# Kernel tuning notes

Measured on AMD Instinct MI355X. Metric: run time of the kernel, lower is better.

## Reference

```python
import jax, jax.numpy as jnp
import numpy as np

B, S, T = 4, 512, 512
D, F, L, H, V = 512, 2048, 6, 8, 32000
HD = D // H


def setup_inputs() -> dict:
    key = jax.random.key(0)
    ks = list(jax.random.split(key, 16))
    it = iter(ks)

    def w(shape, scale=0.02):
        return jax.random.normal(next(it), shape, jnp.float32) * scale

    enc_in = jax.random.randint(next(it), (B, S), 0, V, dtype=jnp.int32)
    dec_in = jax.random.randint(next(it), (B, T), 0, V, dtype=jnp.int32)

    # sinusoidal positional encoding (make_sine_pos_encoding)
    pos = np.arange(S)[:, None].astype(np.float32)
    i = np.arange(D)[None, :].astype(np.float32)
    angle = pos / np.power(10000.0, (2.0 * np.floor(i / 2.0)) / D)
    pe = np.zeros((S, D), np.float32)
    pe[:, 0::2] = np.sin(angle[:, 0::2])
    pe[:, 1::2] = np.cos(angle[:, 1::2])

    return {
        "enc_in": enc_in,
        "dec_in": dec_in,
        "e_embed": w((V, D)),
        "d_embed": w((V, D)),
        "pos_enc": jnp.asarray(pe),
        "enc_mha_W": w((L, 4, D, D)),      # q,k,v,out
        "enc_mha_b": jnp.zeros((L, 4, D), jnp.float32),
        "enc_ln_g": jnp.ones((L, 2, D), jnp.float32),
        "enc_ln_b": jnp.zeros((L, 2, D), jnp.float32),
        "enc_ffn_W1": w((L, D, F)),
        "enc_ffn_b1": jnp.zeros((L, F), jnp.float32),
        "enc_ffn_W2": w((L, F, D)),
        "enc_ffn_b2": jnp.zeros((L, D), jnp.float32),
        "dec_mha_W": w((L, 8, D, D)),      # self q,k,v,out then cross q,k,v,out
        "dec_mha_b": jnp.zeros((L, 8, D), jnp.float32),
        "dec_ln_g": jnp.ones((L, 3, D), jnp.float32),
        "dec_ln_b": jnp.zeros((L, 3, D), jnp.float32),
        "dec_ffn_W1": w((L, D, F)),
        "dec_ffn_b1": jnp.zeros((L, F), jnp.float32),
        "dec_ffn_W2": w((L, F, D)),
        "dec_ffn_b2": jnp.zeros((L, D), jnp.float32),
    }


def _layer_norm(x, g, b, eps=1e-6):
    m = jnp.mean(x, axis=-1, keepdims=True)
    v = jnp.mean(jnp.square(x - m), axis=-1, keepdims=True)
    return (x - m) * jax.lax.rsqrt(v + eps) * g + b


def _split_heads(x):
    b, n, _ = x.shape
    return x.reshape(b, n, H, HD).transpose(0, 2, 1, 3)  # b h n d


def _mha(xq, xkv, W, b, mask):
    # W: [>=4, D, D] slice of (q,k,v,out); mask: broadcastable to [b,h,nq,nk]
    q = _split_heads(xq @ W[0] + b[0])
    k = _split_heads(xkv @ W[1] + b[1])
    v = _split_heads(xkv @ W[2] + b[2])
    s = jnp.einsum('bhqd,bhkd->bhqk', q, k) / jnp.sqrt(jnp.float32(HD))
    s = s + mask * (-1e9)
    a = jax.nn.softmax(s, axis=-1)
    o = jnp.einsum('bhqk,bhkd->bhqd', a, v)
    o = o.transpose(0, 2, 1, 3).reshape(xq.shape[0], xq.shape[1], D)
    return o @ W[3] + b[3]


def _forward(enc_in, dec_in, e_embed, d_embed, pos_enc,
             enc_mha_W, enc_mha_b, enc_ln_g, enc_ln_b,
             enc_ffn_W1, enc_ffn_b1, enc_ffn_W2, enc_ffn_b2,
             dec_mha_W, dec_mha_b, dec_ln_g, dec_ln_b,
             dec_ffn_W1, dec_ffn_b1, dec_ffn_W2, dec_ffn_b2):
    # masks: 1.0 where attention is blocked
    enc_pad = (enc_in == 0).astype(jnp.float32)[:, None, None, :]   # [B,1,1,S]
    dec_pad = (dec_in == 0).astype(jnp.float32)[:, None, None, :]   # [B,1,1,T]
    la = jnp.triu(jnp.ones((T, T), jnp.float32), k=1)[None, None]   # [1,1,T,T]
    look_ahead = jnp.maximum(la, dec_pad)                           # [B,1,T,T]

    scale = jnp.float32(D) ** 0.5
    e = e_embed[enc_in] * scale + pos_enc[None, :S]
    d = d_embed[dec_in] * scale + pos_enc[None, :T]

    for l in range(L):
        y = _mha(e, e, enc_mha_W[l], enc_mha_b[l], enc_pad)
        e = _layer_norm(e + y, enc_ln_g[l, 0], enc_ln_b[l, 0])
        y = jax.nn.relu(e @ enc_ffn_W1[l] + enc_ffn_b1[l]) @ enc_ffn_W2[l] + enc_ffn_b2[l]
        e = _layer_norm(e + y, enc_ln_g[l, 1], enc_ln_b[l, 1])

    for l in range(L):
        y = _mha(d, d, dec_mha_W[l, 0:4], dec_mha_b[l, 0:4], look_ahead)
        d = _layer_norm(d + y, dec_ln_g[l, 0], dec_ln_b[l, 0])
        y = _mha(d, e, dec_mha_W[l, 4:8], dec_mha_b[l, 4:8], enc_pad)
        d = _layer_norm(d + y, dec_ln_g[l, 1], dec_ln_b[l, 1])
        y = jax.nn.relu(d @ dec_ffn_W1[l] + dec_ffn_b1[l]) @ dec_ffn_W2[l] + dec_ffn_b2[l]
        d = _layer_norm(d + y, dec_ln_g[l, 2], dec_ln_b[l, 2])

    return d @ d_embed.T  # [B,T,V] logits


def reference(enc_in, dec_in, e_embed, d_embed, pos_enc,
              enc_mha_W, enc_mha_b, enc_ln_g, enc_ln_b,
              enc_ffn_W1, enc_ffn_b1, enc_ffn_W2, enc_ffn_b2,
              dec_mha_W, dec_mha_b, dec_ln_g, dec_ln_b,
              dec_ffn_W1, dec_ffn_b1, dec_ffn_W2, dec_ffn_b2):
    return _forward(enc_in, dec_in, e_embed, d_embed, pos_enc,
                    enc_mha_W, enc_mha_b, enc_ln_g, enc_ln_b,
                    enc_ffn_W1, enc_ffn_b1, enc_ffn_W2, enc_ffn_b2,
                    dec_mha_W, dec_mha_b, dec_ln_g, dec_ln_b,
                    dec_ffn_W1, dec_ffn_b1, dec_ffn_W2, dec_ffn_b2)
```

## Files before the change

### kernel.cpp

```cpp
#include <hip/hip_runtime.h>
#include <hip/hip_bf16.h>
#include <math.h>

#define B_ 4
#define S_ 512
#define D_ 512
#define F_ 2048
#define L_ 6
#define H_ 8
#define V_ 32000

typedef unsigned short u16;
typedef __attribute__((ext_vector_type(8))) short bhalf8;
typedef __attribute__((ext_vector_type(4))) float f32x4;

__device__ __forceinline__ u16 f2b(float v) {
    unsigned x = __builtin_bit_cast(unsigned, v);
    return (u16)((x + 0x7FFFu + ((x >> 16) & 1u)) >> 16);
}

#define GLD16(g, l) __builtin_amdgcn_global_load_lds( \
    (const __attribute__((address_space(1))) void*)(g), \
    (__attribute__((address_space(3))) void*)(l), 16, 0, 0)

__device__ __forceinline__ float redmax16(float v) {
    #pragma unroll
    for (int m = 1; m < 16; m <<= 1) v = fmaxf(v, __shfl_xor(v, m));
    return v;
}
__device__ __forceinline__ float redsum16(float v) {
    #pragma unroll
    for (int m = 1; m < 16; m <<= 1) v += __shfl_xor(v, m);
    return v;
}

template<int NWR, int NWC, int WM, int WN, int OUT, int RELU, int MLOOP,
         int SPLITA, int XMAJOR, int NT, int VTT>
__global__ __launch_bounds__(NWR * NWC * 64)
void mfma_gemm(const u16* __restrict__ A, const u16* __restrict__ A2, int acut,
               const u16* __restrict__ B,
               const float* __restrict__ bias, void* __restrict__ Cv,
               int K, int lda, int ldb, int ldc,
               u16* __restrict__ vtp, int vc0)
{
    constexpr int BM = NWR * WM, BN = NWC * WN;
    constexpr int NW = NWR * NWC;
    constexpr int CH_A = BM / 16, CH_B = BN / 16, CH = CH_A + CH_B;
    constexpr int NI = WM / 16, NJ = WN / 16;

    __shared__ u16 As[BM * 32];
    __shared__ u16 Bs[BN * 32];
    __shared__ u16 TT[VTT ? 64 * 72 : 8];

    const int tid = threadIdx.x;
    const int wid = tid >> 6, lane = tid & 63;
    const int wrow = wid / NWC, wcol = wid % NWC;
    const long bn = (XMAJOR ? (long)blockIdx.y : (long)blockIdx.x) * BN;
    const long bmbase = (XMAJOR ? (long)blockIdx.x : (long)blockIdx.y);
    const int r4 = lane >> 2, c4 = lane & 3;
    const int l15 = lane & 15, l4 = lane >> 4;

    const u16* Ause = (SPLITA && bn >= acut) ? A2 : A;

    #pragma unroll 1
    for (int mi = 0; mi < MLOOP; ++mi) {
        const long bm = (bmbase * MLOOP + mi) * BM;

        f32x4 acc[NI][NJ];
        #pragma unroll
        for (int i = 0; i < NI; ++i)
            #pragma unroll
            for (int j = 0; j < NJ; ++j)
                acc[i][j] = (f32x4){0.f, 0.f, 0.f, 0.f};

        for (int k0 = 0; k0 < K; k0 += 32) {
            #pragma unroll
            for (int t = 0; t < CH / NW; ++t) {
                int c = wid + t * NW;
                if (c < CH_A) {
                    const u16* g = Ause + (bm + c * 16 + r4) * (long)lda + k0 + c4 * 8;
                    GLD16(g, As + c * 512 + lane * 8);
                } else {
                    int cb = c - CH_A;
                    const u16* g = B + (bn + cb * 16 + r4) * (long)ldb + k0 + c4 * 8;
                    GLD16(g, Bs + cb * 512 + lane * 8);
                }
            }
            __syncthreads();
            bhalf8 af[NI], bfr[NJ];
            #pragma unroll
            for (int i = 0; i < NI; ++i)
                af[i] = *(const bhalf8*)&As[(wrow * WM + i * 16 + l15) * 32 + l4 * 8];
            #pragma unroll
            for (int j = 0; j < NJ; ++j)
                bfr[j] = *(const bhalf8*)&Bs[(wcol * WN + j * 16 + l15) * 32 + l4 * 8];
            #pragma unroll
            for (int i = 0; i < NI; ++i)
                #pragma unroll
                for (int j = 0; j < NJ; ++j)
                    acc[i][j] = __builtin_amdgcn_mfma_f32_16x16x32_bf16(af[i], bfr[j], acc[i][j], 0, 0, 0);
            __syncthreads();
        }

        if (VTT && vtp != nullptr && bn >= vc0) {
            #pragma unroll
            for (int j = 0; j < NJ; ++j) {
                const int c = wcol * WN + j * 16 + l15;
                const float bv = bias ? bias[bn + c] : 0.f;
                #pragma unroll
                for (int i = 0; i < NI; ++i) {
                    const int rw = wrow * WM + i * 16 + (l4 << 2);
                    #pragma unroll
                    for (int r = 0; r < 4; ++r)
                        TT[c * 72 + rw + r] = f2b(acc[i][j][r] + bv);
                }
            }
            __syncthreads();
            {
                const int c = tid >> 1, hh = tid & 1;
                const u16* src = &TT[c * 72 + hh * 32];
                u16* dst = &vtp[(bn - vc0 + c) * 2048 + bm + hh * 32];
                #pragma unroll
                for (int p = 0; p < 4; ++p)
                    *(uint4*)(dst + p * 8) = *(const uint4*)(src + p * 8);
            }
            __syncthreads();
            continue;
        }

        float* Cf = (float*)Cv;
        u16*   Cb = (u16*)Cv;
        const int rowb = wrow * WM + (l4 << 2);
        const int colb = wcol * WN + l15;
        #pragma unroll
        for (int j = 0; j < NJ; ++j) {
            const long gc = bn + colb + j * 16;
            const float bv = bias ? bias[gc] : 0.f;
            #pragma unroll
            for (int i = 0; i < NI; ++i) {
                const long gr = bm + rowb + i * 16;
                #pragma unroll
                for (int r = 0; r < 4; ++r) {
                    float v = acc[i][j][r] + bv;
                    if (RELU) v = fmaxf(v, 0.f);
                    if (OUT == 0) {
                        if (NT) __builtin_nontemporal_store(v, &Cf[(gr + r) * (long)ldc + gc]);
                        else    Cf[(gr + r) * (long)ldc + gc] = v;
                    } else {
                        Cb[(gr + r) * (long)ldc + gc] = f2b(v);
                    }
                }
            }
        }
    }
}

__global__ __launch_bounds__(512)
void gemm_ln_kernel(const u16* __restrict__ A, const u16* __restrict__ B,
                    const float* __restrict__ bias,
                    float* __restrict__ x, u16* __restrict__ xb,
                    const float* __restrict__ g, const float* __restrict__ bb,
                    int K)
{
    __shared__ u16 As[16 * 32];
    __shared__ u16 Bs[512 * 32];
    __shared__ float red[2][16][8];
    __shared__ float mv[2][16];

    const int tid = threadIdx.x, w = tid >> 6, lane = tid & 63;
    const int l15 = lane & 15, l4 = lane >> 4;
    const int r4 = lane >> 2, c4 = lane & 3;
    const long bm = (long)blockIdx.x * 16;

    f32x4 acc[4];
    #pragma unroll
    for (int j = 0; j < 4; ++j) acc[j] = (f32x4){0.f, 0.f, 0.f, 0.f};

    for (int k0 = 0; k0 < K; k0 += 32) {
        #pragma unroll
        for (int t = 0; t < 5; ++t) {
            int c = w + t * 8;
            if (c < 33) {
                if (c == 0) {
                    GLD16(A + (bm + r4) * (long)K + k0 + c4 * 8, As + lane * 8);
                } else {
                    GLD16(B + ((c - 1) * 16 + r4) * (long)K + k0 + c4 * 8,
                          Bs + (c - 1) * 512 + lane * 8);
                }
            }
        }
        __syncthreads();
        bhalf8 af = *(const bhalf8*)&As[l15 * 32 + l4 * 8];
        #pragma unroll
        for (int j = 0; j < 4; ++j) {
            bhalf8 bf = *(const bhalf8*)&Bs[(w * 64 + j * 16 + l15) * 32 + l4 * 8];
            acc[j] = __builtin_amdgcn_mfma_f32_16x16x32_bf16(af, bf, acc[j], 0, 0, 0);
        }
        __syncthreads();
    }

    float vbuf[4][4], s[4] = {0, 0, 0, 0}, s2[4] = {0, 0, 0, 0};
    #pragma unroll
    for (int j = 0; j < 4; ++j) {
        int col = w * 64 + j * 16 + l15;
        float bv = bias[col];
        #pragma unroll
        for (int r = 0; r < 4; ++r) {
            int row = l4 * 4 + r;
            float v = acc[j][r] + bv + x[(bm + row) * 512 + col];
            vbuf[j][r] = v;
            s[r] += v; s2[r] += v * v;
        }
    }
    #pragma unroll
    for (int r = 0; r < 4; ++r) { s[r] = redsum16(s[r]); s2[r] = redsum16(s2[r]); }
    if (l15 == 0) {
        #pragma unroll
        for (int r = 0; r < 4; ++r) {
            red[0][l4 * 4 + r][w] = s[r];
            red[1][l4 * 4 + r][w] = s2[r];
        }
    }
    __syncthreads();
    if (tid < 16) {
        float S = 0.f, S2 = 0.f;
        #pragma unroll
        for (int q = 0; q < 8; ++q) { S += red[0][tid][q]; S2 += red[1][tid][q]; }
        float mean = S * (1.f / 512.f);
        float var = S2 * (1.f / 512.f) - mean * mean;
        mv[0][tid] = mean;
        mv[1][tid] = rsqrtf(var + 1e-6f);
    }
    __syncthreads();
    #pragma unroll
    for (int j = 0; j < 4; ++j) {
        int col = w * 64 + j * 16 + l15;
        float gg = g[col], bbv = bb[col];
        #pragma unroll
        for (int r = 0; r < 4; ++r) {
            int row = l4 * 4 + r;
            float o = (vbuf[j][r] - mv[0][row]) * mv[1][row] * gg + bbv;
            x[(bm + row) * 512 + col] = o;
            xb[(bm + row) * 512 + col] = f2b(o);
        }
    }
}

template<int CAUSAL>
__global__ __launch_bounds__(256)
void flash_kernel(const u16* __restrict__ Qp, int ldq,
                  const u16* __restrict__ Kp, int ldk,
                  const u16* __restrict__ Vt,
                  const int* __restrict__ tok,
                  u16* __restrict__ Op)
{
    __shared__ u16 QS[64 * 64];
    __shared__ u16 KS[64 * 64];
    __shared__ u16 VS[64 * 64];
    __shared__ u16 PS[4 * 16 * 64];
    __shared__ float MK[512];

    const int tid = threadIdx.x, lane = tid & 63, w = tid >> 6;
    const int l15 = lane & 15, l4 = lane >> 4;
    const int qb = blockIdx.x, bh = blockIdx.y;
    const int b = bh >> 3, h = bh & 7;

    const u16* Q = Qp + (long)(b * 512 + qb * 64) * ldq + h * 64;
    const u16* K = Kp + (long)(b * 512) * ldk + h * 64;
    const u16* V = Vt + (long)(h * 64) * 2048 + b * 512;
    u16* O = Op + (long)(b * 512 + qb * 64) * 512 + h * 64;

    {
        int t0 = tok[b * 512 + tid];
        int t1 = tok[b * 512 + 256 + tid];
        MK[tid]       = (t0 == 0) ? -1e9f : 0.f;
        MK[tid + 256] = (t1 == 0) ? -1e9f : 0.f;
    }
    {
        int r = tid >> 3;
        int c = (tid & 7) ^ (r & 7);
        GLD16(Q + (long)r * ldq + c * 8,        QS + tid * 8);
        GLD16(Q + (long)(r + 32) * ldq + c * 8, QS + 2048 + tid * 8);
    }

    f32x4 oacc[4];
    float mrun[4], lrun[4];
    #pragma unroll
    for (int j = 0; j < 4; ++j) oacc[j] = (f32x4){0.f, 0.f, 0.f, 0.f};
    #pragma unroll
    for (int r = 0; r < 4; ++r) { mrun[r] = -1e30f; lrun[r] = 0.f; }

    bhalf8 qa[2];
    const int tmax = CAUSAL ? qb : 7;

    for (int t = 0; t <= tmax; ++t) {
        {
            int r = tid >> 3;
            int c = (tid & 7) ^ (r & 7);
            GLD16(K + (long)(t * 64 + r) * ldk + c * 8,       KS + tid * 8);
            GLD16(K + (long)(t * 64 + 32 + r) * ldk + c * 8,  KS + 2048 + tid * 8);
            GLD16(V + (long)r * 2048 + t * 64 + c * 8,        VS + tid * 8);
            GLD16(V + (long)(r + 32) * 2048 + t * 64 + c * 8, VS + 2048 + tid * 8);
        }
        __syncthreads();
        if (t == 0) {
            #pragma unroll
            for (int kc = 0; kc < 2; ++kc) {
                int row = w * 16 + l15;
                qa[kc] = *(const bhalf8*)&QS[row * 64 + (((kc * 4 + l4) ^ (row & 7)) << 3)];
            }
        }
        f32x4 sac[4];
        #pragma unroll
        for (int jj = 0; jj < 4; ++jj) sac[jj] = (f32x4){0.f, 0.f, 0.f, 0.f};
        bhalf8 kf[4][2];
        #pragma unroll
        for (int jj = 0; jj < 4; ++jj)
            #pragma unroll
            for (int kc = 0; kc < 2; ++kc) {
                int row = jj * 16 + l15;
                kf[jj][kc] = *(const bhalf8*)&KS[row * 64 + (((kc * 4 + l4) ^ (row & 7)) << 3)];
            }
        #pragma unroll
        for (int jj = 0; jj < 4; ++jj)
            #pragma unroll
            for (int kc = 0; kc < 2; ++kc)
                sac[jj] = __builtin_amdgcn_mfma_f32_16x16x32_bf16(qa[kc], kf[jj][kc], sac[jj], 0, 0, 0);

        #pragma unroll
        for (int jj = 0; jj < 4; ++jj) {
            float mk = MK[t * 64 + jj * 16 + l15];
            #pragma unroll
            for (int r = 0; r < 4; ++r) {
                float mk2 = mk;
                if (CAUSAL && t == qb) {
                    int col = t * 64 + jj * 16 + l15;
                    int qr = qb * 64 + w * 16 + l4 * 4 + r;
                    if (col > qr) mk2 = -1e9f;
                }
                sac[jj][r] = sac[jj][r] * 0.125f + mk2;
            }
        }
        #pragma unroll
        for (int r = 0; r < 4; ++r) {
            float mx = fmaxf(fmaxf(sac[0][r], sac[1][r]), fmaxf(sac[2][r], sac[3][r]));
            mx = redmax16(mx);
            float mnew = fmaxf(mrun[r], mx);
            float alpha = __expf(mrun[r] - mnew);
            float sum = 0.f;
            int row_p = l4 * 4 + r;
            #pragma unroll
            for (int jj = 0; jj < 4; ++jj) {
                float pv = __expf(sac[jj][r] - mnew);
                sum += pv;
                int kv = jj * 16 + l15;
                PS[w * 1024 + row_p * 64 + ((((kv >> 3) ^ (row_p & 7)) << 3) | (kv & 7))] = f2b(pv);
            }
            sum = redsum16(sum);
            lrun[r] = lrun[r] * alpha + sum;
            mrun[r] = mnew;
            #pragma unroll
            for (int jd = 0; jd < 4; ++jd) oacc[jd][r] *= alpha;
        }
        bhalf8 pa[2], vf[4][2];
        #pragma unroll
        for (int kc = 0; kc < 2; ++kc) {
            int row = l15;
            pa[kc] = *(const bhalf8*)&PS[w * 1024 + row * 64 + (((kc * 4 + l4) ^ (row & 7)) << 3)];
        }
        #pragma unroll
        for (int jd = 0; jd < 4; ++jd)
            #pragma unroll
            for (int kc = 0; kc < 2; ++kc) {
                int row = jd * 16 + l15;
                vf[jd][kc] = *(const bhalf8*)&VS[row * 64 + (((kc * 4 + l4) ^ (row & 7)) << 3)];
            }
        #pragma unroll
        for (int jd = 0; jd < 4; ++jd)
            #pragma unroll
            for (int kc = 0; kc < 2; ++kc)
                oacc[jd] = __builtin_amdgcn_mfma_f32_16x16x32_bf16(pa[kc], vf[jd][kc], oacc[jd], 0, 0, 0);
        __syncthreads();
    }

    #pragma unroll
    for (int r = 0; r < 4; ++r) {
        float inv = 1.f / lrun[r];
        int row = w * 16 + l4 * 4 + r;
        #pragma unroll
        for (int jd = 0; jd < 4; ++jd)
            O[(long)row * 512 + jd * 16 + l15] = f2b(oacc[jd][r] * inv);
    }
}

__global__ __launch_bounds__(256)
void transpose_many(const float* __restrict__ inA, const float* __restrict__ inB,
                    int zsplit, int R, int C, u16* __restrict__ out)
{
    int z = blockIdx.z;
    const float* in = (z < zsplit) ? inA + (long)z * R * C
                                   : inB + (long)(z - zsplit) * R * C;
    u16* o = out + (long)z * R * C;
    __shared__ float tb[64][65];
    const int tr = blockIdx.y * 64, tc = blockIdx.x * 64;
    const int col = threadIdx.x & 63, r0 = threadIdx.x >> 6;
    #pragma unroll
    for (int p = 0; p < 16; ++p) {
        int row = r0 * 16 + p;
        tb[row][col] = in[(long)(tr + row) * C + tc + col];
    }
    __syncthreads();
    #pragma unroll
    for (int p = 0; p < 16; ++p) {
        int row = r0 * 16 + p;
        o[(long)(tc + row) * R + tr + col] = f2b(tb[col][row]);
    }
}

__global__ __launch_bounds__(256)
void convert_b16(const float4* __restrict__ in, u16* __restrict__ out, long n4)
{
    long i = (long)blockIdx.x * 256 + threadIdx.x;
    if (i >= n4) return;
    float4 v = in[i];
    uint2 p;
    p.x = (unsigned)f2b(v.x) | ((unsigned)f2b(v.y) << 16);
    p.y = (unsigned)f2b(v.z) | ((unsigned)f2b(v.w) << 16);
    *(uint2*)(out + i * 4) = p;
}

__global__ __launch_bounds__(256)
void embed_kernel(const int* __restrict__ tE, const int* __restrict__ tD,
                  const float* __restrict__ eE, const float* __restrict__ eD,
                  const float* __restrict__ pos,
                  float* __restrict__ xE, float* __restrict__ xD,
                  u16* __restrict__ bE, u16* __restrict__ bD, float scale)
{
    const int z = blockIdx.y;
    const int* tok = z ? tD : tE;
    const float* emb = z ? eD : eE;
    float* x = z ? xD : xE;
    u16* xb = z ? bD : bE;
    int row = blockIdx.x;
    int s = row & (S_ - 1);
    int t = tok[row];
    const float* er = emb + (long)t * D_;
    const float* pr = pos + (long)s * D_;
    float* o = x + (long)row * D_;
    u16*  ob = xb + (long)row * D_;
    int i = threadIdx.x;
    float v0 = er[i]       * scale + pr[i];
    float v1 = er[i + 256] * scale + pr[i + 256];
    o[i] = v0;        o[i + 256] = v1;
    ob[i] = f2b(v0);  ob[i + 256] = f2b(v1);
}

__global__ __launch_bounds__(256)
void add_ln_kernel(float* __restrict__ x, const float* __restrict__ y,
                   u16* __restrict__ xb,
                   const float* __restrict__ g, const float* __restrict__ bb)
{
    long row = blockIdx.x;
    float* xr = x + row * D_;
    u16* xo = xb + row * D_;
    const float* yr = y + row * D_;
    int t = threadIdx.x, t2 = t + 256;

    float r0 = xr[t] + yr[t];
    float r1 = xr[t2] + yr[t2];
    float s = r0 + r1;
    float s2 = r0 * r0 + r1 * r1;
    #pragma unroll
    for (int i = 1; i < 64; i <<= 1) {
        s  += __shfl_xor(s, i);
        s2 += __shfl_xor(s2, i);
    }
    __shared__ float rs[4], rs2[4];
    int wid = t >> 6;
    if ((t & 63) == 0) { rs[wid] = s; rs2[wid] = s2; }
    __syncthreads();
    s  = rs[0] + rs[1] + rs[2] + rs[3];
    s2 = rs2[0] + rs2[1] + rs2[2] + rs2[3];

    float mean = s * (1.f / D_);
    float var  = s2 * (1.f / D_) - mean * mean;
    float inv  = rsqrtf(var + 1e-6f);
    float o0 = (r0 - mean) * inv * g[t]  + bb[t];
    float o1 = (r1 - mean) * inv * g[t2] + bb[t2];
    xr[t] = o0;       xr[t2] = o1;
    xo[t] = f2b(o0);  xo[t2] = f2b(o1);
}

extern "C" void kernel_launch(void* const* d_in, const int* in_sizes, int n_in,
                              void* d_out, int out_size, void* d_ws, size_t ws_size,
                              hipStream_t stream)
{
    const int*   enc_in     = (const int*)  d_in[0];
    const int*   dec_in     = (const int*)  d_in[1];
    const float* e_embed    = (const float*)d_in[2];
    const float* d_embed    = (const float*)d_in[3];
    const float* pos_enc    = (const float*)d_in[4];
    const float* enc_mha_W  = (const float*)d_in[5];
    const float* enc_mha_b  = (const float*)d_in[6];
    const float* enc_ln_g   = (const float*)d_in[7];
    const float* enc_ln_b   = (const float*)d_in[8];
    const float* enc_ffn_W1 = (const float*)d_in[9];
    const float* enc_ffn_b1 = (const float*)d_in[10];
    const float* enc_ffn_W2 = (const float*)d_in[11];
    const float* enc_ffn_b2 = (const float*)d_in[12];
    const float* dec_mha_W  = (const float*)d_in[13];
    const float* dec_mha_b  = (const float*)d_in[14];
    const float* dec_ln_g   = (const float*)d_in[15];
    const float* dec_ln_b   = (const float*)d_in[16];
    const float* dec_ffn_W1 = (const float*)d_in[17];
    const float* dec_ffn_b1 = (const float*)d_in[18];
    const float* dec_ffn_W2 = (const float*)d_in[19];
    const float* dec_ffn_b2 = (const float*)d_in[20];
    float* out = (float*)d_out;

    const int  BS  = B_ * S_;
    const long BSD = (long)BS * D_;
    const long DD  = (long)D_ * D_;
    const long DF  = (long)D_ * F_;

    char* p = (char*)d_ws;
    auto alloc = [&](long bytes) { char* r = p; p += (bytes + 255) & ~255L; return r; };
    float* e    = (float*)alloc(BSD * 4);
    float* dd   = (float*)alloc(BSD * 4);
    float* y    = (float*)alloc(BSD * 4);
    u16*   eb   = (u16*)  alloc(BSD * 2);
    u16*   ddb  = (u16*)  alloc(BSD * 2);
    u16*   qkv  = (u16*)  alloc((long)BS * 1536 * 2);
    u16*   att  = (u16*)  alloc(BSD * 2);
    u16*   vt   = (u16*)  alloc(BSD * 2);
    u16*   ffnh = (u16*)  alloc((long)BS * F_ * 2);
    u16*   wEmb = (u16*)  alloc((long)V_ * D_ * 2);
    u16*   wMha = (u16*)  alloc(72 * DD * 2);
    u16*   wF1  = (u16*)  alloc(12 * DF * 2);
    u16*   wF2  = (u16*)  alloc(12 * DF * 2);

    transpose_many<<<dim3(8, 8, 72), 256, 0, stream>>>(enc_mha_W, dec_mha_W, 24, 512, 512, wMha);
    transpose_many<<<dim3(32, 8, 12), 256, 0, stream>>>(enc_ffn_W1, dec_ffn_W1, 6, 512, 2048, wF1);
    transpose_many<<<dim3(8, 32, 12), 256, 0, stream>>>(enc_ffn_W2, dec_ffn_W2, 6, 2048, 512, wF2);
    convert_b16<<<16000, 256, 0, stream>>>((const float4*)d_embed, wEmb, (long)V_ * D_ / 4);

    const float scale = sqrtf((float)D_);
    embed_kernel<<<dim3(BS, 2), 256, 0, stream>>>(enc_in, dec_in, e_embed, d_embed,
                                                  pos_enc, e, dd, eb, ddb, scale);

    #define GEMM_BIG(grid, RELU, OUTT, A, Bp, bias, C, K, lda, ldb, ldc) \
        mfma_gemm<2,2,64,64,OUTT,RELU,1,0,0,0,0><<<grid, 256, 0, stream>>>(A, A, 1 << 30, Bp, bias, C, K, lda, ldb, ldc, nullptr, 0)
    #define GEMM_SKV(grid, A, Bp, bias, C, K, lda, ldb, ldc, vtp, vc0) \
        mfma_gemm<2,1,32,64,1,0,1,0,0,0,1><<<grid, 128, 0, stream>>>(A, A, 1 << 30, Bp, bias, C, K, lda, ldb, ldc, vtp, vc0)
    #define GEMM_SK(grid, OUTT, A, Bp, bias, C, K, lda, ldb, ldc) \
        mfma_gemm<2,1,32,64,OUTT,0,1,0,0,0,0><<<grid, 128, 0, stream>>>(A, A, 1 << 30, Bp, bias, C, K, lda, ldb, ldc, nullptr, 0)

    for (int l = 0; l < L_; ++l) {
        const u16* Wl = wMha + (long)l * 4 * DD;
        const float* bl = enc_mha_b + (long)l * 4 * D_;
        GEMM_SKV(dim3(24, 32), eb, Wl, bl, qkv, 512, 512, 512, 1536, vt, 1024);
        flash_kernel<0><<<dim3(8, 32), 256, 0, stream>>>(qkv, 1536, qkv + 512, 1536, vt, enc_in, att);
        gemm_ln_kernel<<<128, 512, 0, stream>>>(att, Wl + 3 * DD, bl + 3 * D_,
            e, eb, enc_ln_g + (long)(l * 2) * D_, enc_ln_b + (long)(l * 2) * D_, 512);
        GEMM_BIG(dim3(16, 16), 1, 1, eb, wF1 + (long)l * DF, enc_ffn_b1 + (long)l * F_,
                 ffnh, 512, 512, 512, 2048);
        GEMM_SK(dim3(8, 32), 0, ffnh, wF2 + (long)l * DF, enc_ffn_b2 + (long)l * D_,
                y, 2048, 2048, 2048, 512);
        add_ln_kernel<<<BS, 256, 0, stream>>>(e, y, eb,
            enc_ln_g + (long)(l * 2 + 1) * D_, enc_ln_b + (long)(l * 2 + 1) * D_);
    }

    for (int l = 0; l < L_; ++l) {
        const u16* Wl = wMha + (long)(24 + l * 8) * DD;
        const float* bl = dec_mha_b + (long)l * 8 * D_;
        GEMM_SKV(dim3(24, 32), ddb, Wl, bl, qkv, 512, 512, 512, 1536, vt, 1024);
        flash_kernel<1><<<dim3(8, 32), 256, 0, stream>>>(qkv, 1536, qkv + 512, 1536, vt, dec_in, att);
        gemm_ln_kernel<<<128, 512, 0, stream>>>(att, Wl + 3 * DD, bl + 3 * D_,
            dd, ddb, dec_ln_g + (long)(l * 3) * D_, dec_ln_b + (long)(l * 3) * D_, 512);
        mfma_gemm<2,1,32,64,1,0,1,1,0,0,1><<<dim3(24, 32), 128, 0, stream>>>(
            ddb, eb, 512, Wl + 4 * DD, bl + 4 * D_, qkv,
            512, 512, 512, 1536, vt, 1024);
        flash_kernel<0><<<dim3(8, 32), 256, 0, stream>>>(qkv, 1536, qkv + 512, 1536, vt, enc_in, att);
        gemm_ln_kernel<<<128, 512, 0, stream>>>(att, Wl + 7 * DD, bl + 7 * D_,
            dd, ddb, dec_ln_g + (long)(l * 3 + 1) * D_, dec_ln_b + (long)(l * 3 + 1) * D_, 512);
        GEMM_BIG(dim3(16, 16), 1, 1, ddb, wF1 + (long)(6 + l) * DF, dec_ffn_b1 + (long)l * F_,
                 ffnh, 512, 512, 512, 2048);
        GEMM_SK(dim3(8, 32), 0, ffnh, wF2 + (long)(6 + l) * DF, dec_ffn_b2 + (long)l * D_,
                y, 2048, 2048, 2048, 512);
        add_ln_kernel<<<BS, 256, 0, stream>>>(dd, y, ddb,
            dec_ln_g + (long)(l * 3 + 2) * D_, dec_ln_b + (long)(l * 3 + 2) * D_);
    }

    mfma_gemm<2,2,64,64,0,0,1,0,1,1,0><<<dim3(16, 250), 256, 0, stream>>>(
        ddb, ddb, 1 << 30, wEmb, nullptr, out, 512, 512, 512, 32000, nullptr, 0);
}
```

Measured before the change: 1.805 ms.

## Double-buffer LDS tiles in GEMM and flash attention; swizzle logits GEMM grid

Both the generic MFMA GEMM and the flash-attention kernel now use two LDS buffers. The next K tile (or next K/V block) is fetched with global_load_lds while MFMAs run on the current one, which removes one barrier per iteration and overlaps loads with compute. The final vocab-projection GEMM moves to a 1D grid with an XCD-aware swizzle that maps consecutive blocks onto shared N tiles, aiming to improve L2 reuse of embedding rows across the 8 XCDs. The cost is doubled LDS usage, which may reduce occupancy. Correctness relies on the single barrier per iteration ordering the reads of the previous buffer before it is overwritten.

```diff
diff --git a/kernel.cpp b/kernel.cpp
--- a/kernel.cpp
+++ b/kernel.cpp
@@ -35,7 +35,7 @@
 }
 
 template<int NWR, int NWC, int WM, int WN, int OUT, int RELU, int MLOOP,
-         int SPLITA, int XMAJOR, int NT, int VTT>
+         int SPLITA, int XMAJOR, int NT, int VTT, int SWZ>
 __global__ __launch_bounds__(NWR * NWC * 64)
 void mfma_gemm(const u16* __restrict__ A, const u16* __restrict__ A2, int acut,
                const u16* __restrict__ B,
@@ -48,15 +48,24 @@
     constexpr int CH_A = BM / 16, CH_B = BN / 16, CH = CH_A + CH_B;
     constexpr int NI = WM / 16, NJ = WN / 16;
 
-    __shared__ u16 As[BM * 32];
-    __shared__ u16 Bs[BN * 32];
+    __shared__ u16 As[2][BM * 32];
+    __shared__ u16 Bs[2][BN * 32];
     __shared__ u16 TT[VTT ? 64 * 72 : 8];
 
     const int tid = threadIdx.x;
     const int wid = tid >> 6, lane = tid & 63;
     const int wrow = wid / NWC, wcol = wid % NWC;
-    const long bn = (XMAJOR ? (long)blockIdx.y : (long)blockIdx.x) * BN;
-    const long bmbase = (XMAJOR ? (long)blockIdx.x : (long)blockIdx.y);
+    long bn, bmbase;
+    if (SWZ) {
+        long b0 = blockIdx.x;
+        long per = (long)gridDim.x >> 3;
+        long w = (b0 & 7) * per + (b0 >> 3);
+        bn = (w >> 4) * BN;
+        bmbase = w & 15;
+    } else {
+        bn = (XMAJOR ? (long)blockIdx.y : (long)blockIdx.x) * BN;
+        bmbase = (XMAJOR ? (long)blockIdx.x : (long)blockIdx.y);
+    }
     const int r4 = lane >> 2, c4 = lane & 3;
     const int l15 = lane & 15, l4 = lane >> 4;
 
@@ -73,33 +82,49 @@
             for (int j = 0; j < NJ; ++j)
                 acc[i][j] = (f32x4){0.f, 0.f, 0.f, 0.f};
 
+        #pragma unroll
+        for (int t = 0; t < CH / NW; ++t) {
+            int c = wid + t * NW;
+            if (c < CH_A) {
+                GLD16(Ause + (bm + c * 16 + r4) * (long)lda + c4 * 8,
+                      &As[0][c * 512 + lane * 8]);
+            } else {
+                int cb = c - CH_A;
+                GLD16(B + (bn + cb * 16 + r4) * (long)ldb + c4 * 8,
+                      &Bs[0][cb * 512 + lane * 8]);
+            }
+        }
+
         for (int k0 = 0; k0 < K; k0 += 32) {
-            #pragma unroll
-            for (int t = 0; t < CH / NW; ++t) {
-                int c = wid + t * NW;
-                if (c < CH_A) {
-                    const u16* g = Ause + (bm + c * 16 + r4) * (long)lda + k0 + c4 * 8;
-                    GLD16(g, As + c * 512 + lane * 8);
-                } else {
-                    int cb = c - CH_A;
-                    const u16* g = B + (bn + cb * 16 + r4) * (long)ldb + k0 + c4 * 8;
-                    GLD16(g, Bs + cb * 512 + lane * 8);
+            const int cur = (k0 >> 5) & 1;
+            __syncthreads();
+            if (k0 + 32 < K) {
+                const int kn = k0 + 32;
+                #pragma unroll
+                for (int t = 0; t < CH / NW; ++t) {
+                    int c = wid + t * NW;
+                    if (c < CH_A) {
+                        GLD16(Ause + (bm + c * 16 + r4) * (long)lda + kn + c4 * 8,
+                              &As[cur ^ 1][c * 512 + lane * 8]);
+                    } else {
+                        int cb = c - CH_A;
+                        GLD16(B + (bn + cb * 16 + r4) * (long)ldb + kn + c4 * 8,
+                              &Bs[cur ^ 1][cb * 512 + lane * 8]);
+                    }
                 }
             }
-            __syncthreads();
             bhalf8 af[NI], bfr[NJ];
             #pragma unroll
             for (int i = 0; i < NI; ++i)
-                af[i] = *(const bhalf8*)&As[(wrow * WM + i * 16 + l15) * 32 + l4 * 8];
+                af[i] = *(const bhalf8*)&As[cur][(wrow * WM + i * 16 + l15) * 32 + l4 * 8];
             #pragma unroll
             for (int j = 0; j < NJ; ++j)
-                bfr[j] = *(const bhalf8*)&Bs[(wcol * WN + j * 16 + l15) * 32 + l4 * 8];
+                bfr[j] = *(const bhalf8*)&Bs[cur][(wcol * WN + j * 16 + l15) * 32 + l4 * 8];
             #pragma unroll
             for (int i = 0; i < NI; ++i)
                 #pragma unroll
                 for (int j = 0; j < NJ; ++j)
                     acc[i][j] = __builtin_amdgcn_mfma_f32_16x16x32_bf16(af[i], bfr[j], acc[i][j], 0, 0, 0);
-            __syncthreads();
         }
 
         if (VTT && vtp != nullptr && bn >= vc0) {
@@ -255,8 +280,8 @@
                   u16* __restrict__ Op)
 {
     __shared__ u16 QS[64 * 64];
-    __shared__ u16 KS[64 * 64];
-    __shared__ u16 VS[64 * 64];
+    __shared__ u16 KS[2][64 * 64];
+    __shared__ u16 VS[2][64 * 64];
     __shared__ u16 PS[4 * 16 * 64];
     __shared__ float MK[512];
 
@@ -276,11 +301,23 @@
         MK[tid]       = (t0 == 0) ? -1e9f : 0.f;
         MK[tid + 256] = (t1 == 0) ? -1e9f : 0.f;
     }
+    const int r = tid >> 3;
+    const int c = (tid & 7) ^ (r & 7);
     {
-        int r = tid >> 3;
-        int c = (tid & 7) ^ (r & 7);
         GLD16(Q + (long)r * ldq + c * 8,        QS + tid * 8);
         GLD16(Q + (long)(r + 32) * ldq + c * 8, QS + 2048 + tid * 8);
+        GLD16(K + (long)r * ldk + c * 8,              KS[0] + tid * 8);
+        GLD16(K + (long)(32 + r) * ldk + c * 8,       KS[0] + 2048 + tid * 8);
+        GLD16(V + (long)r * 2048 + c * 8,             VS[0] + tid * 8);
+        GLD16(V + (long)(r + 32) * 2048 + c * 8,      VS[0] + 2048 + tid * 8);
+    }
+    __syncthreads();
+
+    bhalf8 qa[2];
+    #pragma unroll
+    for (int kc = 0; kc < 2; ++kc) {
+        int row = w * 16 + l15;
+        qa[kc] = *(const bhalf8*)&QS[row * 64 + (((kc * 4 + l4) ^ (row & 7)) << 3)];
     }
 
     f32x4 oacc[4];
@@ -288,27 +325,18 @@
     #pragma unroll
     for (int j = 0; j < 4; ++j) oacc[j] = (f32x4){0.f, 0.f, 0.f, 0.f};
     #pragma unroll
-    for (int r = 0; r < 4; ++r) { mrun[r] = -1e30f; lrun[r] = 0.f; }
-
-    bhalf8 qa[2];
+    for (int rr = 0; rr < 4; ++rr) { mrun[rr] = -1e30f; lrun[rr] = 0.f; }
+
     const int tmax = CAUSAL ? qb : 7;
 
     for (int t = 0; t <= tmax; ++t) {
-        {
-            int r = tid >> 3;
-            int c = (tid & 7) ^ (r & 7);
-            GLD16(K + (long)(t * 64 + r) * ldk + c * 8,       KS + tid * 8);
-            GLD16(K + (long)(t * 64 + 32 + r) * ldk + c * 8,  KS + 2048 + tid * 8);
-            GLD16(V + (long)r * 2048 + t * 64 + c * 8,        VS + tid * 8);
-            GLD16(V + (long)(r + 32) * 2048 + t * 64 + c * 8, VS + 2048 + tid * 8);
-        }
-        __syncthreads();
-        if (t == 0) {
-            #pragma unroll
-            for (int kc = 0; kc < 2; ++kc) {
-                int row = w * 16 + l15;
-                qa[kc] = *(const bhalf8*)&QS[row * 64 + (((kc * 4 + l4) ^ (row & 7)) << 3)];
-            }
+        const int cur = t & 1;
+        if (t < tmax) {
+            const int tn = t + 1;
+            GLD16(K + (long)(tn * 64 + r) * ldk + c * 8,        KS[cur ^ 1] + tid * 8);
+            GLD16(K + (long)(tn * 64 + 32 + r) * ldk + c * 8,   KS[cur ^ 1] + 2048 + tid * 8);
+            GLD16(V + (long)r * 2048 + tn * 64 + c * 8,         VS[cur ^ 1] + tid * 8);
+            GLD16(V + (long)(r + 32) * 2048 + tn * 64 + c * 8,  VS[cur ^ 1] + 2048 + tid * 8);
         }
         f32x4 sac[4];
         #pragma unroll
@@ -319,7 +347,7 @@
             #pragma unroll
             for (int kc = 0; kc < 2; ++kc) {
                 int row = jj * 16 + l15;
-                kf[jj][kc] = *(const bhalf8*)&KS[row * 64 + (((kc * 4 + l4) ^ (row & 7)) << 3)];
+                kf[jj][kc] = *(const bhalf8*)&KS[cur][row * 64 + (((kc * 4 + l4) ^ (row & 7)) << 3)];
             }
         #pragma unroll
         for (int jj = 0; jj < 4; ++jj)
@@ -331,36 +359,36 @@
         for (int jj = 0; jj < 4; ++jj) {
             float mk = MK[t * 64 + jj * 16 + l15];
             #pragma unroll
-            for (int r = 0; r < 4; ++r) {
+            for (int rr = 0; rr < 4; ++rr) {
                 float mk2 = mk;
                 if (CAUSAL && t == qb) {
                     int col = t * 64 + jj * 16 + l15;
-                    int qr = qb * 64 + w * 16 + l4 * 4 + r;
+                    int qr = qb * 64 + w * 16 + l4 * 4 + rr;
                     if (col > qr) mk2 = -1e9f;
                 }
-                sac[jj][r] = sac[jj][r] * 0.125f + mk2;
-            }
-        }
-        #pragma unroll
-        for (int r = 0; r < 4; ++r) {
-            float mx = fmaxf(fmaxf(sac[0][r], sac[1][r]), fmaxf(sac[2][r], sac[3][r]));
+                sac[jj][rr] = sac[jj][rr] * 0.125f + mk2;
+            }
+        }
+        #pragma unroll
+        for (int rr = 0; rr < 4; ++rr) {
+            float mx = fmaxf(fmaxf(sac[0][rr], sac[1][rr]), fmaxf(sac[2][rr], sac[3][rr]));
             mx = redmax16(mx);
-            float mnew = fmaxf(mrun[r], mx);
-            float alpha = __expf(mrun[r] - mnew);
+            float mnew = fmaxf(mrun[rr], mx);
+            float alpha = __expf(mrun[rr] - mnew);
             float sum = 0.f;
-            int row_p = l4 * 4 + r;
+            int row_p = l4 * 4 + rr;
             #pragma unroll
             for (int jj = 0; jj < 4; ++jj) {
-                float pv = __expf(sac[jj][r] - mnew);
+                float pv = __expf(sac[jj][rr] - mnew);
                 sum += pv;
                 int kv = jj * 16 + l15;
                 PS[w * 1024 + row_p * 64 + ((((kv >> 3) ^ (row_p & 7)) << 3) | (kv & 7))] = f2b(pv);
             }
             sum = redsum16(sum);
-            lrun[r] = lrun[r] * alpha + sum;
-            mrun[r] = mnew;
-            #pragma unroll
-            for (int jd = 0; jd < 4; ++jd) oacc[jd][r] *= alpha;
+            lrun[rr] = lrun[rr] * alpha + sum;
+            mrun[rr] = mnew;
+            #pragma unroll
+            for (int jd = 0; jd < 4; ++jd) oacc[jd][rr] *= alpha;
         }
         bhalf8 pa[2], vf[4][2];
         #pragma unroll
@@ -373,7 +401,7 @@
             #pragma unroll
             for (int kc = 0; kc < 2; ++kc) {
                 int row = jd * 16 + l15;
-                vf[jd][kc] = *(const bhalf8*)&VS[row * 64 + (((kc * 4 + l4) ^ (row & 7)) << 3)];
+                vf[jd][kc] = *(const bhalf8*)&VS[cur][row * 64 + (((kc * 4 + l4) ^ (row & 7)) << 3)];
             }
         #pragma unroll
         for (int jd = 0; jd < 4; ++jd)
@@ -384,12 +412,12 @@
     }
 
     #pragma unroll
-    for (int r = 0; r < 4; ++r) {
-        float inv = 1.f / lrun[r];
-        int row = w * 16 + l4 * 4 + r;
+    for (int rr = 0; rr < 4; ++rr) {
+        float inv = 1.f / lrun[rr];
+        int row = w * 16 + l4 * 4 + rr;
         #pragma unroll
         for (int jd = 0; jd < 4; ++jd)
-            O[(long)row * 512 + jd * 16 + l15] = f2b(oacc[jd][r] * inv);
+            O[(long)row * 512 + jd * 16 + l15] = f2b(oacc[jd][rr] * inv);
     }
 }
 
@@ -549,11 +577,11 @@
                                                   pos_enc, e, dd, eb, ddb, scale);
 
     #define GEMM_BIG(grid, RELU, OUTT, A, Bp, bias, C, K, lda, ldb, ldc) \
-        mfma_gemm<2,2,64,64,OUTT,RELU,1,0,0,0,0><<<grid, 256, 0, stream>>>(A, A, 1 << 30, Bp, bias, C, K, lda, ldb, ldc, nullptr, 0)
+        mfma_gemm<2,2,64,64,OUTT,RELU,1,0,0,0,0,0><<<grid, 256, 0, stream>>>(A, A, 1 << 30, Bp, bias, C, K, lda, ldb, ldc, nullptr, 0)
     #define GEMM_SKV(grid, A, Bp, bias, C, K, lda, ldb, ldc, vtp, vc0) \
-        mfma_gemm<2,1,32,64,1,0,1,0,0,0,1><<<grid, 128, 0, stream>>>(A, A, 1 << 30, Bp, bias, C, K, lda, ldb, ldc, vtp, vc0)
+        mfma_gemm<2,1,32,64,1,0,1,0,0,0,1,0><<<grid, 128, 0, stream>>>(A, A, 1 << 30, Bp, bias, C, K, lda, ldb, ldc, vtp, vc0)
     #define GEMM_SK(grid, OUTT, A, Bp, bias, C, K, lda, ldb, ldc) \
-        mfma_gemm<2,1,32,64,OUTT,0,1,0,0,0,0><<<grid, 128, 0, stream>>>(A, A, 1 << 30, Bp, bias, C, K, lda, ldb, ldc, nullptr, 0)
+        mfma_gemm<2,1,32,64,OUTT,0,1,0,0,0,0,0><<<grid, 128, 0, stream>>>(A, A, 1 << 30, Bp, bias, C, K, lda, ldb, ldc, nullptr, 0)
 
     for (int l = 0; l < L_; ++l) {
         const u16* Wl = wMha + (long)l * 4 * DD;
@@ -577,7 +605,7 @@
         flash_kernel<1><<<dim3(8, 32), 256, 0, stream>>>(qkv, 1536, qkv + 512, 1536, vt, dec_in, att);
         gemm_ln_kernel<<<128, 512, 0, stream>>>(att, Wl + 3 * DD, bl + 3 * D_,
             dd, ddb, dec_ln_g + (long)(l * 3) * D_, dec_ln_b + (long)(l * 3) * D_, 512);
-        mfma_gemm<2,1,32,64,1,0,1,1,0,0,1><<<dim3(24, 32), 128, 0, stream>>>(
+        mfma_gemm<2,1,32,64,1,0,1,1,0,0,1,0><<<dim3(24, 32), 128, 0, stream>>>(
             ddb, eb, 512, Wl + 4 * DD, bl + 4 * D_, qkv,
             512, 512, 512, 1536, vt, 1024);
         flash_kernel<0><<<dim3(8, 32), 256, 0, stream>>>(qkv, 1536, qkv + 512, 1536, vt, enc_in, att);
@@ -591,6 +619,6 @@
             dec_ln_g + (long)(l * 3 + 2) * D_, dec_ln_b + (long)(l * 3 + 2) * D_);
     }
 
-    mfma_gemm<2,2,64,64,0,0,1,0,1,1,0><<<dim3(16, 250), 256, 0, stream>>>(
+    mfma_gemm<2,2,64,64,0,0,1,0,0,1,0,1><<<dim3(4000), 256, 0, stream>>>(
         ddb, ddb, 1 << 30, wEmb, nullptr, out, 512, 512, 512, 32000, nullptr, 0);
 }
```

After: 1.791 ms. No clear change (-0.8%).
